# Optimization experiments

Measured on AMD Instinct MI355X. Metric: run time of the kernel, lower is better.

## Reference

```python
import jax, jax.numpy as jnp
import numpy as np

OUT_DIM = 4096
DPC = 16
N = OUT_DIM * DPC  # 65536
BATCH = 512


def setup_inputs() -> dict:
    key = jax.random.key(0)
    k1, k2 = jax.random.split(key)
    x = jax.random.normal(k1, (BATCH, N), dtype=jnp.float32)
    duty_cycle = jax.random.uniform(k2, (N,), dtype=jnp.float32)
    boost_strength = jnp.ones((1,), dtype=jnp.float32)
    return {"x": x, "duty_cycle": duty_cycle, "boost_strength": boost_strength}


def reference(x, duty_cycle, boost_strength):
    # GenericKWinners.forward in training mode (k = out_dim), boost_strength > 0.
    n = x.shape[1]
    target_density = OUT_DIM / n
    bs = boost_strength[0]
    boost_factors = jnp.exp((target_density - duty_cycle) * bs)  # [N]
    # x is detached in the original before boosting/masking
    boosted = jax.lax.stop_gradient(x) * boost_factors  # [B, N]
    # Overlapping windows: group k covers [k*(dpc-1), k*(dpc-1)+dpc)
    starts = jnp.arange(OUT_DIM) * (DPC - 1)  # [OUT_DIM]
    win_idx = starts[:, None] + jnp.arange(DPC)[None, :]  # [OUT_DIM, DPC]
    windows = boosted[:, win_idx]  # [B, OUT_DIM, DPC]
    ind = jnp.argmax(windows, axis=-1)  # [B, OUT_DIM]
    mask = jax.nn.one_hot(ind, DPC, dtype=x.dtype)  # [B, OUT_DIM, DPC]
    mask = mask.reshape(x.shape[0], OUT_DIM * DPC)  # [B, N]
    return mask * x
```

## Files before the change

kernel.cpp:

```cpp
#include <hip/hip_runtime.h>

#define OUT_DIM 4096
#define DPC     16
#define NCOL    65536
#define BATCH   512
#define NWAVE   32768

typedef float nvec4 __attribute__((ext_vector_type(4)));

__global__ void boost_table_kernel(const float* __restrict__ duty,
                                   const float* __restrict__ bs_ptr,
                                   float* __restrict__ bf) {
    int p = blockIdx.x * blockDim.x + threadIdx.x;
    if (p < NCOL) {
        float t = (0.0625f - duty[p]) * bs_ptr[0];
        bf[p] = (float)exp((double)t);
    }
}

__global__ __launch_bounds__(256, 8) void dkw_kernel(const float* __restrict__ x,
                                                     const float* __restrict__ bf,
                                                     float* __restrict__ out) {
    __shared__ float sb[4][1024];
    __shared__ int   sj[4][64];

    const int lane = threadIdx.x & 63;
    const int wv   = threadIdx.x >> 6;
    const int gw   = blockIdx.x * 4 + wv;
    const int row  = gw >> 6;
    const int wc   = gw & 63;
    const int rowbase = row << 16;

    const int in_off = wc * 960;
    const float4* __restrict__ xg   = (const float4*)(x + rowbase + in_off);
    const float4* __restrict__ bg   = (const float4*)(bf + in_off);
    const float4* __restrict__ xo_g = (const float4*)(x + rowbase + (wc << 10));
    float4* __restrict__ sb4 = (float4*)sb[wv];
    #pragma unroll
    for (int r = 0; r < 4; ++r) {
        const int i = lane + 64 * r;
        float4 a = xg[i];
        float4 b = bg[i];
        float4 p;
        p.x = a.x * b.x; p.y = a.y * b.y; p.z = a.z * b.z; p.w = a.w * b.w;
        sb4[i] = p;
    }
    float4 xo0 = xo_g[lane];
    float4 xo1 = xo_g[lane + 64];
    float4 xo2 = xo_g[lane + 128];
    float4 xo3 = xo_g[lane + 192];
    asm volatile("" ::: "memory");

    {
        const float* __restrict__ p = sb[wv] + lane * 15;
        float best = p[0];
        int   bj   = 0;
        #pragma unroll
        for (int k = 1; k < DPC; ++k) {
            float v = p[k];
            if (v > best) { best = v; bj = k; }
        }
        sj[wv][lane] = bj;
    }
    asm volatile("" ::: "memory");

    float4* __restrict__ og = (float4*)(out + rowbase + (wc << 10));
    const float4 xoarr[4] = {xo0, xo1, xo2, xo3};
    #pragma unroll
    for (int r = 0; r < 4; ++r) {
        const int i  = lane + 64 * r;
        const int w  = i >> 2;
        const int jm = sj[wv][w];
        const float4 v = xoarr[r];
        const int j0 = (i & 3) << 2;
        float4 o;
        o.x = (j0     == jm) ? v.x : 0.0f;
        o.y = (j0 + 1 == jm) ? v.y : 0.0f;
        o.z = (j0 + 2 == jm) ? v.z : 0.0f;
        o.w = (j0 + 3 == jm) ? v.w : 0.0f;
        __builtin_nontemporal_store(*(const nvec4*)&o, (nvec4*)&og[i]);
    }
}

extern "C" void kernel_launch(void* const* d_in, const int* in_sizes, int n_in,
                              void* d_out, int out_size, void* d_ws, size_t ws_size,
                              hipStream_t stream) {
    const float* x    = (const float*)d_in[0];
    const float* duty = (const float*)d_in[1];
    const float* bs   = (const float*)d_in[2];
    float* out = (float*)d_out;
    float* bf  = (float*)d_ws;

    hipLaunchKernelGGL(boost_table_kernel, dim3(NCOL / 256), dim3(256), 0, stream,
                       duty, bs, bf);
    hipLaunchKernelGGL(dkw_kernel, dim3(NWAVE / 4), dim3(256), 0, stream,
                       x, bf, out);
}
```

Baseline: 237.3 us.

## Stage input slabs into LDS via direct global-to-LDS loads with larger blocks

Each 512-thread block now handles a quarter of a row, loading the whole input span (plus overlap) into LDS with global_load_lds, instead of each wave reading its window twice from global (once for boosting and once for the output pass). Output values are read back from LDS before the span is boosted in place, and winner indices are stored as bytes. This removes duplicated global reads of x but adds several block-wide barriers and a large LDS footprint (about 77KB) that limits occupancy to one or two blocks per CU.

```diff
diff --git a/kernel.cpp b/kernel.cpp
--- a/kernel.cpp
+++ b/kernel.cpp
@@ -4,7 +4,6 @@
 #define DPC     16
 #define NCOL    65536
 #define BATCH   512
-#define NWAVE   32768
 
 typedef float nvec4 __attribute__((ext_vector_type(4)));
 
@@ -18,67 +17,74 @@
     }
 }
 
-__global__ __launch_bounds__(256, 8) void dkw_kernel(const float* __restrict__ x,
+__global__ __launch_bounds__(512, 4) void dkw_kernel(const float* __restrict__ x,
                                                      const float* __restrict__ bf,
                                                      float* __restrict__ out) {
-    __shared__ float sb[4][1024];
-    __shared__ int   sj[4][64];
+    __shared__ float sx[19456];
+    __shared__ unsigned char sjb[1024];
 
-    const int lane = threadIdx.x & 63;
-    const int wv   = threadIdx.x >> 6;
-    const int gw   = blockIdx.x * 4 + wv;
-    const int row  = gw >> 6;
-    const int wc   = gw & 63;
-    const int rowbase = row << 16;
+    const int tid = threadIdx.x;
+    const int r   = blockIdx.x >> 2;
+    const int b   = blockIdx.x & 3;
+    const int rowbase = r << 16;
+    const int span_f  = b * 15360;
+    const int S4      = 4096 + (b << 8);
 
-    const int in_off = wc * 960;
-    const float4* __restrict__ xg   = (const float4*)(x + rowbase + in_off);
-    const float4* __restrict__ bg   = (const float4*)(bf + in_off);
-    const float4* __restrict__ xo_g = (const float4*)(x + rowbase + (wc << 10));
-    float4* __restrict__ sb4 = (float4*)sb[wv];
+    const float4* __restrict__ xg4 = (const float4*)(x + rowbase + span_f);
+    float4* sx4 = (float4*)sx;
+
+    for (int i = tid; i < S4; i += 512) {
+        __builtin_amdgcn_global_load_lds(
+            (const __attribute__((address_space(1))) void*)(xg4 + i),
+            (__attribute__((address_space(3))) void*)(sx4 + i), 16, 0, 0);
+    }
+    __syncthreads();
+
+    float4 xo[8];
     #pragma unroll
-    for (int r = 0; r < 4; ++r) {
-        const int i = lane + 64 * r;
-        float4 a = xg[i];
-        float4 b = bg[i];
-        float4 p;
-        p.x = a.x * b.x; p.y = a.y * b.y; p.z = a.z * b.z; p.w = a.w * b.w;
-        sb4[i] = p;
-    }
-    float4 xo0 = xo_g[lane];
-    float4 xo1 = xo_g[lane + 64];
-    float4 xo2 = xo_g[lane + 128];
-    float4 xo3 = xo_g[lane + 192];
-    asm volatile("" ::: "memory");
+    for (int k = 0; k < 8; ++k)
+        xo[k] = sx4[(b << 8) + tid + (k << 9)];
+    __syncthreads();
 
     {
-        const float* __restrict__ p = sb[wv] + lane * 15;
+        const float4* __restrict__ bg4 = (const float4*)(bf + span_f);
+        for (int i = tid; i < 3844; i += 512) {
+            float4 a = sx4[i];
+            float4 c = bg4[i];
+            a.x *= c.x; a.y *= c.y; a.z *= c.z; a.w *= c.w;
+            sx4[i] = a;
+        }
+    }
+    __syncthreads();
+
+    #pragma unroll
+    for (int m = 0; m < 2; ++m) {
+        const int w = tid + (m << 9);
+        const float* __restrict__ p = sx + w * 15;
         float best = p[0];
         int   bj   = 0;
         #pragma unroll
-        for (int k = 1; k < DPC; ++k) {
-            float v = p[k];
-            if (v > best) { best = v; bj = k; }
+        for (int kk = 1; kk < DPC; ++kk) {
+            float v = p[kk];
+            if (v > best) { best = v; bj = kk; }
         }
-        sj[wv][lane] = bj;
+        sjb[w] = (unsigned char)bj;
     }
-    asm volatile("" ::: "memory");
+    __syncthreads();
 
-    float4* __restrict__ og = (float4*)(out + rowbase + (wc << 10));
-    const float4 xoarr[4] = {xo0, xo1, xo2, xo3};
+    float4* __restrict__ og4 = (float4*)(out + rowbase + (b << 14));
     #pragma unroll
-    for (int r = 0; r < 4; ++r) {
-        const int i  = lane + 64 * r;
-        const int w  = i >> 2;
-        const int jm = sj[wv][w];
-        const float4 v = xoarr[r];
-        const int j0 = (i & 3) << 2;
+    for (int k = 0; k < 8; ++k) {
+        const int o4 = tid + (k << 9);
+        const int jm = (int)sjb[o4 >> 2];
+        const int j0 = (o4 & 3) << 2;
+        const float4 v = xo[k];
         float4 o;
         o.x = (j0     == jm) ? v.x : 0.0f;
         o.y = (j0 + 1 == jm) ? v.y : 0.0f;
         o.z = (j0 + 2 == jm) ? v.z : 0.0f;
         o.w = (j0 + 3 == jm) ? v.w : 0.0f;
-        __builtin_nontemporal_store(*(const nvec4*)&o, (nvec4*)&og[i]);
+        __builtin_nontemporal_store(*(const nvec4*)&o, (nvec4*)&og4[o4]);
     }
 }
 
@@ -93,6 +99,6 @@
 
     hipLaunchKernelGGL(boost_table_kernel, dim3(NCOL / 256), dim3(256), 0, stream,
                        duty, bs, bf);
-    hipLaunchKernelGGL(dkw_kernel, dim3(NWAVE / 4), dim3(256), 0, stream,
+    hipLaunchKernelGGL(dkw_kernel, dim3(BATCH * 4), dim3(512), 0, stream,
                        x, bf, out);
 }
```

New measurement: 243.8 us. 1.03x slower.

## Split fused winners/mask kernel into winner-index pass and streaming mask pass

Applied to the files above, without the earlier changes.

Replaces the single fused kernel with two kernels. The first computes per-window argmax indices into a byte buffer in workspace. The second streams x with eight float4 loads per thread and writes the masked output. This aims to raise memory-level parallelism in the output pass, at the cost of an extra launch and losing on-chip reuse of x between the argmax and masking steps. It falls back to the fused kernel if the workspace is too small.

```diff
diff --git a/kernel.cpp b/kernel.cpp
--- a/kernel.cpp
+++ b/kernel.cpp
@@ -5,6 +5,7 @@
 #define NCOL    65536
 #define BATCH   512
 #define NWAVE   32768
+#define NF4     8388608
 
 typedef float nvec4 __attribute__((ext_vector_type(4)));
 
@@ -15,6 +16,72 @@
     if (p < NCOL) {
         float t = (0.0625f - duty[p]) * bs_ptr[0];
         bf[p] = (float)exp((double)t);
+    }
+}
+
+__global__ __launch_bounds__(256, 8) void winners_kernel(const float* __restrict__ x,
+                                                         const float* __restrict__ bf,
+                                                         unsigned char* __restrict__ sj) {
+    __shared__ float sb[4][1024];
+
+    const int lane = threadIdx.x & 63;
+    const int wv   = threadIdx.x >> 6;
+    const int gw   = blockIdx.x * 4 + wv;
+    const int row  = gw >> 6;
+    const int wc   = gw & 63;
+    const int rowbase = row << 16;
+
+    const int in_off = wc * 960;
+    const float4* __restrict__ xg = (const float4*)(x + rowbase + in_off);
+    const float4* __restrict__ bg = (const float4*)(bf + in_off);
+    float4* __restrict__ sb4 = (float4*)sb[wv];
+    #pragma unroll
+    for (int r = 0; r < 4; ++r) {
+        const int i = lane + 64 * r;
+        float4 a = xg[i];
+        float4 b = bg[i];
+        float4 p;
+        p.x = a.x * b.x; p.y = a.y * b.y; p.z = a.z * b.z; p.w = a.w * b.w;
+        sb4[i] = p;
+    }
+    asm volatile("" ::: "memory");
+
+    const float* __restrict__ p = sb[wv] + lane * 15;
+    float best = p[0];
+    int   bj   = 0;
+    #pragma unroll
+    for (int k = 1; k < DPC; ++k) {
+        float v = p[k];
+        if (v > best) { best = v; bj = k; }
+    }
+    sj[(gw << 6) + lane] = (unsigned char)bj;
+}
+
+__global__ __launch_bounds__(256, 8) void mask_kernel(const float* __restrict__ x,
+                                                      const unsigned char* __restrict__ sj,
+                                                      float* __restrict__ out) {
+    const int t = blockIdx.x * 256 + threadIdx.x;
+    const float4* __restrict__ x4 = (const float4*)x;
+    float4* __restrict__ o4 = (float4*)out;
+
+    float4 v[8];
+    int    jm[8];
+    #pragma unroll
+    for (int k = 0; k < 8; ++k) {
+        const int j = t + (k << 20);
+        v[k]  = x4[j];
+        jm[k] = (int)sj[j >> 2];
+    }
+    #pragma unroll
+    for (int k = 0; k < 8; ++k) {
+        const int j  = t + (k << 20);
+        const int j0 = (j & 3) << 2;
+        float4 o;
+        o.x = (jm[k] == j0    ) ? v[k].x : 0.0f;
+        o.y = (jm[k] == j0 + 1) ? v[k].y : 0.0f;
+        o.z = (jm[k] == j0 + 2) ? v[k].z : 0.0f;
+        o.w = (jm[k] == j0 + 3) ? v[k].w : 0.0f;
+        __builtin_nontemporal_store(*(const nvec4*)&o, (nvec4*)&o4[j]);
     }
 }
 
@@ -90,9 +157,18 @@
     const float* bs   = (const float*)d_in[2];
     float* out = (float*)d_out;
     float* bf  = (float*)d_ws;
+    unsigned char* sj = (unsigned char*)d_ws + NCOL * sizeof(float);
 
     hipLaunchKernelGGL(boost_table_kernel, dim3(NCOL / 256), dim3(256), 0, stream,
                        duty, bs, bf);
-    hipLaunchKernelGGL(dkw_kernel, dim3(NWAVE / 4), dim3(256), 0, stream,
-                       x, bf, out);
+
+    if (ws_size >= NCOL * sizeof(float) + (size_t)(BATCH * OUT_DIM)) {
+        hipLaunchKernelGGL(winners_kernel, dim3(NWAVE / 4), dim3(256), 0, stream,
+                           x, bf, sj);
+        hipLaunchKernelGGL(mask_kernel, dim3(NF4 / 8 / 256), dim3(256), 0, stream,
+                           x, sj, out);
+    } else {
+        hipLaunchKernelGGL(dkw_kernel, dim3(NWAVE / 4), dim3(256), 0, stream,
+                           x, bf, out);
+    }
 }
```

New measurement: 259.4 us. +9.3%, slower.
